# Kernel tuning notes

Measured on AMD Instinct MI355X. Metric: run time of the kernel, lower is better.

The kernel has to match this reference:

```python
import jax, jax.numpy as jnp
import numpy as np

NUM_CLASSES = 10
PGD_NUMS = 10
ALPHA = 0.15
# Hardcoded in the original module: sign vector for 10 classes
SIGN_VEC = jnp.array([-1.0] * 4 + [1.0] * 6, dtype=jnp.float32)


def setup_inputs() -> dict:
    key = jax.random.key(0)
    k1, k2, k3 = jax.random.split(key, 3)
    B = 1048576
    logit = jax.random.normal(k1, (B, NUM_CLASSES), dtype=jnp.float32)
    y = jax.random.randint(k2, (B,), 0, NUM_CLASSES, dtype=jnp.int32)
    label_freq = jax.random.randint(k3, (NUM_CLASSES,), 0, PGD_NUMS, dtype=jnp.int32)
    return {"logit": logit, "y": y, "label_freq": label_freq}


def _compute_adv(logit, y):
    # softmax over classes, then per-class mean of softmax rows (one-hot^T @ p)
    p = jax.nn.softmax(logit, axis=-1)  # [B, C]
    sum_class_logit = jax.ops.segment_sum(p, y, num_segments=NUM_CLASSES)  # [C, C]
    counts = jax.ops.segment_sum(jnp.ones(y.shape[0], dtype=logit.dtype), y,
                                 num_segments=NUM_CLASSES)  # [C]
    counts = jnp.where(counts == 0, jnp.asarray(100.0, logit.dtype), counts)
    mean_class_logit = sum_class_logit / counts[:, None]  # [C, C]
    grad = mean_class_logit - jnp.eye(NUM_CLASSES, dtype=logit.dtype)
    # Faithful to torch: norm over dim=0 (columns), then reshape(-1,1) divides row i
    col_norm = jnp.linalg.norm(grad, axis=0)  # [C]
    grad = grad / col_norm[:, None]
    grad = ALPHA * grad * SIGN_VEC[:, None].astype(logit.dtype)
    return grad[y]  # index_select along dim 0 -> [B, C]


def reference(logit, y, label_freq):
    logit_copy = logit

    def step(l, _):
        l_new = l + _compute_adv(l, y)
        return l_new, l_new

    _, logit_steps = jax.lax.scan(step, logit, None, length=PGD_NUMS)  # [P, B, C]

    # Original: logit_news = sum_i logit_steps[label_freq[i]] * (y == i)
    # Since class masks are disjoint, this is a per-sample gather of step label_freq[y[n]].
    steps_per_sample = label_freq[y]  # [B]
    B = logit.shape[0]
    logit_news = logit_steps[steps_per_sample, jnp.arange(B)]  # [B, C]

    # mean cross-entropy
    log_p = jax.nn.log_softmax(logit_news, axis=-1)
    loss_adv = -jnp.mean(jnp.take_along_axis(log_p, y[:, None].astype(jnp.int32), axis=1))
    return loss_adv, logit_news, logit_copy
```

## Files before the change

kernel.cpp:

```cpp
#include <hip/hip_runtime.h>
#include <hip/hip_cooperative_groups.h>

#define PGD   10
#define ALPHA 0.15f
#define NTAB  32
#define NSUB  8

#define FTH   512
#define FSP   4
#define FTS   (FTH * FSP)

#define NTHR  256
#define SPT   4
#define TSAMP (NTHR * SPT)

#define WS_COUNTS 0
#define WS_STAB   320
#define WS_DGLOB  32320
#define WS_BAR    33320
#define WS_ZERO_N 33324

__global__ void k_init(float* __restrict__ ws, float* __restrict__ out) {
    int i = blockIdx.x * blockDim.x + threadIdx.x;
    if (i == 0) out[0] = 0.f;
    int gs = gridDim.x * blockDim.x;
    for (int k = i; k < WS_ZERO_N; k += gs) ws[k] = 0.f;
}

__device__ __forceinline__ float aload(const float* p) {
    return __hip_atomic_load(p, __ATOMIC_RELAXED, __HIP_MEMORY_SCOPE_AGENT);
}

__device__ __forceinline__ void table_phase(
    const float* __restrict__ Sg, const float* __restrict__ counts_tab,
    const float* Dprev, float* shT, float* shCnt, float* shCn,
    float* shD_out, int tid)
{
    if (tid < 10) {
        float s = 0.f;
        #pragma unroll
        for (int k = 0; k < NTAB; ++k) s += counts_tab[k * 10 + tid];
        shCnt[tid] = (s == 0.f) ? 100.f : s;
    }
    if (tid < 100) {
        float s = 0.f;
        #pragma unroll
        for (int k = 0; k < NTAB; ++k) s += Sg[k * 100 + tid];
        shT[tid] = s;
    }
    __syncthreads();
    if (tid < 100) {
        int c = tid / 10, j = tid - c * 10;
        shT[tid] = shT[tid] / shCnt[c] - ((c == j) ? 1.f : 0.f);
    }
    __syncthreads();
    if (tid < 10) {
        float s = 0.f;
        for (int cc = 0; cc < 10; ++cc) { float g = shT[cc * 10 + tid]; s += g * g; }
        shCn[tid] = sqrtf(s);
    }
    __syncthreads();
    if (tid < 100) {
        int c = tid / 10;
        float sign = (c < 4) ? -1.f : 1.f;
        float g = shT[tid] / shCn[c] * (ALPHA * sign);
        shD_out[tid] = (Dprev ? Dprev[tid] : 0.f) + g;
    }
    __syncthreads();
}

__device__ __forceinline__ void load4(const float* __restrict__ logit,
                                      const int* __restrict__ y,
                                      int s0, int B, float* a, int* yc) {
    if (s0 + 4 <= B) {
        const float4* rp = reinterpret_cast<const float4*>(logit + (size_t)s0 * 10);
        float4 q[10];
        #pragma unroll
        for (int i = 0; i < 10; ++i) q[i] = rp[i];
        int4 yv = *reinterpret_cast<const int4*>(y + s0);
        #pragma unroll
        for (int i = 0; i < 10; ++i) {
            a[4 * i + 0] = q[i].x; a[4 * i + 1] = q[i].y;
            a[4 * i + 2] = q[i].z; a[4 * i + 3] = q[i].w;
        }
        yc[0] = yv.x; yc[1] = yv.y; yc[2] = yv.z; yc[3] = yv.w;
    } else {
        #pragma unroll
        for (int k = 0; k < 4; ++k) {
            int idx = s0 + k;
            if (idx < B) {
                yc[k] = y[idx];
                for (int j = 0; j < 10; ++j) a[k * 10 + j] = logit[(size_t)idx * 10 + j];
            } else {
                yc[k] = -1;
                for (int j = 0; j < 10; ++j) a[k * 10 + j] = 0.f;
            }
        }
    }
}

__global__ __launch_bounds__(FTH, 2) void k_fused(
    const float* __restrict__ logit, const int* __restrict__ y,
    const int* __restrict__ label_freq,
    float* __restrict__ out, float* __restrict__ ws, int B)
{
    __shared__ float tile[1024 * 10];
    __shared__ float Dall[PGD][100];
    __shared__ float shT[100];
    __shared__ float shCnt[10];
    __shared__ float shCn[10];
    __shared__ float wtab[NSUB][100];
    __shared__ float ctab[NSUB][10];
    __shared__ int   lf[10];
    __shared__ float wsum[8];

    const int tid = threadIdx.x;
    float* counts_tab = ws + WS_COUNTS;
    float* S_tab      = ws + WS_STAB;
    int*   bar        = (int*)(ws + WS_BAR);

    const size_t ftot = (size_t)B * 10;
    float* news_out = out + 1;
    float* copy_out = out + 1 + ftot;

    if (tid < 10) lf[tid] = label_freq[tid];

    const int s0 = (blockIdx.x * FTH + tid) * FSP;
    float a[40];
    int   yc[4];
    load4(logit, y, s0, B, a, yc);

    const size_t fbase = (size_t)blockIdx.x * (FTS * 10);
    #pragma unroll
    for (int i = 0; i < 10; ++i) {
        size_t fi = fbase + (size_t)(tid + i * FTH) * 4;
        if (fi + 4 <= ftot) {
            float4 v = *reinterpret_cast<const float4*>(logit + fi);
            *reinterpret_cast<float4*>(copy_out + fi) = v;
        } else {
            for (size_t e = fi; e < ftot; ++e) copy_out[e] = logit[e];
        }
    }

    const int nblk = gridDim.x;

    for (int t = 1; t <= PGD; ++t) {
        for (int i = tid; i < NSUB * 100; i += FTH) (&wtab[0][0])[i] = 0.f;
        if (t == 1) for (int i = tid; i < NSUB * 10; i += FTH) (&ctab[0][0])[i] = 0.f;
        __syncthreads();

        const int sub = ((tid >> 6) << 1) | (tid & 1);
        #pragma unroll
        for (int k = 0; k < FSP; ++k) {
            int c = yc[k];
            if (c < 0) continue;
            float tv[10];
            #pragma unroll
            for (int j = 0; j < 10; ++j) tv[j] = a[k * 10 + j];
            if (t >= 2) {
                #pragma unroll
                for (int j = 0; j < 10; ++j) tv[j] += Dall[t - 2][c * 10 + j];
            }
            float m = tv[0];
            #pragma unroll
            for (int j = 1; j < 10; ++j) m = fmaxf(m, tv[j]);
            float s = 0.f;
            #pragma unroll
            for (int j = 0; j < 10; ++j) { tv[j] = __expf(tv[j] - m); s += tv[j]; }
            float r = 1.f / s;
            #pragma unroll
            for (int j = 0; j < 10; ++j) unsafeAtomicAdd(&wtab[sub][c * 10 + j], tv[j] * r);
            if (t == 1) unsafeAtomicAdd(&ctab[sub][c], 1.f);
        }
        __syncthreads();

        const int tb = blockIdx.x & (NTAB - 1);
        if (tid < 100) {
            float s = 0.f;
            #pragma unroll
            for (int w = 0; w < NSUB; ++w) s += wtab[w][tid];
            atomicAdd(&S_tab[(size_t)(t - 1) * (NTAB * 100) + (size_t)tb * 100 + tid], s);
        }
        if (t == 1 && tid < 10) {
            float s = 0.f;
            #pragma unroll
            for (int w = 0; w < NSUB; ++w) s += ctab[w][tid];
            atomicAdd(&counts_tab[tb * 10 + tid], s);
        }

        __syncthreads();
        if (tid == 0) {
            __hip_atomic_fetch_add(bar, 1, __ATOMIC_ACQ_REL, __HIP_MEMORY_SCOPE_AGENT);
            while (__hip_atomic_load(bar, __ATOMIC_ACQUIRE, __HIP_MEMORY_SCOPE_AGENT) < nblk * t)
                __builtin_amdgcn_s_sleep(16);
        }
        __syncthreads();

        if (tid < 10) {
            float s = 0.f;
            #pragma unroll
            for (int k = 0; k < NTAB; ++k) s += aload(&counts_tab[k * 10 + tid]);
            shCnt[tid] = (s == 0.f) ? 100.f : s;
        }
        if (tid < 100) {
            float s = 0.f;
            const float* Sg = S_tab + (size_t)(t - 1) * (NTAB * 100);
            #pragma unroll
            for (int k = 0; k < NTAB; ++k) s += aload(&Sg[k * 100 + tid]);
            shT[tid] = s;
        }
        __syncthreads();
        if (tid < 100) {
            int c = tid / 10, j = tid - c * 10;
            shT[tid] = shT[tid] / shCnt[c] - ((c == j) ? 1.f : 0.f);
        }
        __syncthreads();
        if (tid < 10) {
            float s = 0.f;
            for (int cc = 0; cc < 10; ++cc) { float g = shT[cc * 10 + tid]; s += g * g; }
            shCn[tid] = sqrtf(s);
        }
        __syncthreads();
        if (tid < 100) {
            int c = tid / 10;
            float sign = (c < 4) ? -1.f : 1.f;
            float g = shT[tid] / shCn[c] * (ALPHA * sign);
            Dall[t - 1][tid] = ((t >= 2) ? Dall[t - 2][tid] : 0.f) + g;
        }
        __syncthreads();
    }

    float acc = 0.f;
    for (int cc = 0; cc < 2; ++cc) {
        __syncthreads();
        if ((tid >> 8) == cc) {
            const int lt = tid & 255;
            #pragma unroll
            for (int k = 0; k < FSP; ++k) {
                int c = yc[k];
                if (c < 0) continue;
                int rrel = lt * FSP + k;
                int sel = lf[c];
                float nv[10];
                #pragma unroll
                for (int j = 0; j < 10; ++j) nv[j] = a[k * 10 + j] + Dall[sel][c * 10 + j];
                #pragma unroll
                for (int j = 0; j < 10; ++j) tile[rrel * 10 + j] = nv[j];
                float m = nv[0];
                #pragma unroll
                for (int j = 1; j < 10; ++j) m = fmaxf(m, nv[j]);
                float s = 0.f;
                #pragma unroll
                for (int j = 0; j < 10; ++j) s += __expf(nv[j] - m);
                acc += __logf(s) + m - nv[c];
            }
        }
        __syncthreads();
        const float4* tp = reinterpret_cast<const float4*>(tile);
        #pragma unroll
        for (int i = 0; i < 5; ++i) {
            size_t fo = fbase + (size_t)cc * 10240 + (size_t)(tid + i * FTH) * 4;
            if (fo + 4 <= ftot) {
                *reinterpret_cast<float4*>(news_out + fo) = tp[tid + i * FTH];
            } else {
                size_t lbase = fbase + (size_t)cc * 10240;
                for (size_t e = fo; e < ftot; ++e) news_out[e] = tile[e - lbase];
            }
        }
    }

    #pragma unroll
    for (int off = 32; off > 0; off >>= 1) acc += __shfl_down(acc, off);
    if ((tid & 63) == 0) wsum[tid >> 6] = acc;
    __syncthreads();
    if (tid == 0) {
        float b = 0.f;
        #pragma unroll
        for (int w = 0; w < 8; ++w) b += wsum[w];
        atomicAdd(out, b / (float)B);
    }
}

__global__ __launch_bounds__(NTHR) void k_step(
    const float* __restrict__ logit, const int* __restrict__ y,
    float* __restrict__ ws, int B, int t)
{
    __shared__ float sh_D[100];
    __shared__ float shT[100];
    __shared__ float shCnt[10];
    __shared__ float shCn[10];
    __shared__ float wtab[NSUB][100];
    __shared__ float ctab[NSUB][10];

    const int tid = threadIdx.x;
    float* counts_tab = ws + WS_COUNTS;
    float* S_tab      = ws + WS_STAB;
    float* D_glob     = ws + WS_DGLOB;

    const int s0 = (blockIdx.x * NTHR + tid) * SPT;
    float a[40];
    int   yc[4];
    load4(logit, y, s0, B, a, yc);

    for (int i = tid; i < NSUB * 100; i += NTHR) (&wtab[0][0])[i] = 0.f;
    if (t == 1) for (int i = tid; i < NSUB * 10; i += NTHR) (&ctab[0][0])[i] = 0.f;

    if (t >= 2) {
        table_phase(S_tab + (size_t)(t - 2) * (NTAB * 100), counts_tab,
                    (t >= 3) ? (D_glob + (size_t)(t - 3) * 100) : nullptr,
                    shT, shCnt, shCn, sh_D, tid);
        if (blockIdx.x == 0 && tid < 100) D_glob[(size_t)(t - 2) * 100 + tid] = sh_D[tid];
    }
    __syncthreads();

    const int sub = ((tid >> 6) << 1) | (tid & 1);
    #pragma unroll
    for (int k = 0; k < SPT; ++k) {
        int c = yc[k];
        if (c < 0) continue;
        float tv[10];
        #pragma unroll
        for (int j = 0; j < 10; ++j) tv[j] = a[k * 10 + j];
        if (t >= 2) {
            #pragma unroll
            for (int j = 0; j < 10; ++j) tv[j] += sh_D[c * 10 + j];
        }
        float m = tv[0];
        #pragma unroll
        for (int j = 1; j < 10; ++j) m = fmaxf(m, tv[j]);
        float s = 0.f;
        #pragma unroll
        for (int j = 0; j < 10; ++j) { tv[j] = __expf(tv[j] - m); s += tv[j]; }
        float r = 1.f / s;
        #pragma unroll
        for (int j = 0; j < 10; ++j) unsafeAtomicAdd(&wtab[sub][c * 10 + j], tv[j] * r);
        if (t == 1) unsafeAtomicAdd(&ctab[sub][c], 1.f);
    }
    __syncthreads();

    const int tb = blockIdx.x & (NTAB - 1);
    if (tid < 100) {
        float s = 0.f;
        #pragma unroll
        for (int w = 0; w < NSUB; ++w) s += wtab[w][tid];
        unsafeAtomicAdd(&S_tab[(size_t)(t - 1) * (NTAB * 100) + (size_t)tb * 100 + tid], s);
    }
    if (t == 1 && tid < 10) {
        float s = 0.f;
        #pragma unroll
        for (int w = 0; w < NSUB; ++w) s += ctab[w][tid];
        unsafeAtomicAdd(&counts_tab[tb * 10 + tid], s);
    }
}

__global__ __launch_bounds__(NTHR) void k_final(
    const float* __restrict__ logit, const int* __restrict__ y,
    const int* __restrict__ label_freq,
    float* __restrict__ out, float* __restrict__ ws, int B)
{
    __shared__ float tile_f[TSAMP * 10];
    __shared__ int   yt[TSAMP];
    __shared__ float Dall[PGD][100];
    __shared__ float shT[100];
    __shared__ float shCnt[10];
    __shared__ float shCn[10];
    __shared__ int   lf[10];
    __shared__ float wsum[4];

    const int tid = threadIdx.x;
    float* counts_tab = ws + WS_COUNTS;
    float* S_tab      = ws + WS_STAB;
    float* D_glob     = ws + WS_DGLOB;

    const size_t fbase = (size_t)blockIdx.x * (TSAMP * 10);
    const size_t ftot  = (size_t)B * 10;
    float4 q[10];
    int4 yq;
    #pragma unroll
    for (int i = 0; i < 10; ++i) {
        size_t fi = fbase + (size_t)(tid + i * NTHR) * 4;
        if (fi + 4 <= ftot) {
            q[i] = *reinterpret_cast<const float4*>(logit + fi);
        } else {
            float e[4];
            #pragma unroll
            for (int e2 = 0; e2 < 4; ++e2) e[e2] = (fi + e2 < ftot) ? logit[fi + e2] : 0.f;
            q[i] = make_float4(e[0], e[1], e[2], e[3]);
        }
    }
    {
        int yi = blockIdx.x * TSAMP + tid * 4;
        if (yi + 4 <= B) {
            yq = *reinterpret_cast<const int4*>(y + yi);
        } else {
            yq.x = (yi < B) ? y[yi] : 0;
            yq.y = (yi + 1 < B) ? y[yi + 1] : 0;
            yq.z = (yi + 2 < B) ? y[yi + 2] : 0;
            yq.w = (yi + 3 < B) ? y[yi + 3] : 0;
        }
    }

    table_phase(S_tab + (size_t)9 * (NTAB * 100), counts_tab, D_glob + 8 * 100,
                shT, shCnt, shCn, &Dall[9][0], tid);
    for (int i = tid; i < 900; i += NTHR) Dall[i / 100][i % 100] = D_glob[i];
    if (tid < 10) lf[tid] = label_freq[tid];

    float4* tp = reinterpret_cast<float4*>(tile_f);
    #pragma unroll
    for (int i = 0; i < 10; ++i) tp[tid + i * NTHR] = q[i];
    reinterpret_cast<int4*>(yt)[tid] = yq;
    __syncthreads();

    const int vfloat = (int)((ftot - fbase < (size_t)(TSAMP * 10)) ? (ftot - fbase)
                                                                   : (size_t)(TSAMP * 10));
    float* news_out = out + 1;
    float* copy_out = out + 1 + ftot;

    for (int m = tid; m < vfloat; m += NTHR) copy_out[fbase + m] = tile_f[m];
    __syncthreads();

    float acc = 0.f;
    #pragma unroll
    for (int k = 0; k < SPT; ++k) {
        int sl = tid + k * NTHR;
        int gi = blockIdx.x * TSAMP + sl;
        if (gi >= B) break;
        int c = yt[sl];
        int sel = lf[c];
        float2* rp = reinterpret_cast<float2*>(tile_f + sl * 10);
        float nv[10];
        #pragma unroll
        for (int h = 0; h < 5; ++h) {
            float2 v = rp[h];
            nv[2 * h]     = v.x + Dall[sel][c * 10 + 2 * h];
            nv[2 * h + 1] = v.y + Dall[sel][c * 10 + 2 * h + 1];
        }
        #pragma unroll
        for (int h = 0; h < 5; ++h) rp[h] = make_float2(nv[2 * h], nv[2 * h + 1]);
        float m = nv[0];
        #pragma unroll
        for (int j = 1; j < 10; ++j) m = fmaxf(m, nv[j]);
        float s = 0.f;
        #pragma unroll
        for (int j = 0; j < 10; ++j) s += __expf(nv[j] - m);
        acc += __logf(s) + m - nv[c];
    }
    __syncthreads();

    for (int m = tid; m < vfloat; m += NTHR) news_out[fbase + m] = tile_f[m];

    #pragma unroll
    for (int off = 32; off > 0; off >>= 1) acc += __shfl_down(acc, off);
    if ((tid & 63) == 0) wsum[tid >> 6] = acc;
    __syncthreads();
    if (tid == 0)
        unsafeAtomicAdd(out, (wsum[0] + wsum[1] + wsum[2] + wsum[3]) / (float)B);
}

extern "C" void kernel_launch(void* const* d_in, const int* in_sizes, int n_in,
                              void* d_out, int out_size, void* d_ws, size_t ws_size,
                              hipStream_t stream) {
    const float* logit = (const float*)d_in[0];
    const int*   yy    = (const int*)d_in[1];
    const int*   lf    = (const int*)d_in[2];
    float* out = (float*)d_out;
    float* ws  = (float*)d_ws;
    int B = in_sizes[0] / 10;

    int fblocks = (B + FTS - 1) / FTS;

    int dev = 0; hipGetDevice(&dev);
    int numCU = 0;
    hipDeviceGetAttribute(&numCU, hipDeviceAttributeMultiprocessorCount, dev);
    int maxB = 0;
    hipOccupancyMaxActiveBlocksPerMultiprocessor(&maxB, (const void*)k_fused, FTH, 0);
    bool coop_ok = (maxB > 0) && ((long)maxB * (long)numCU >= (long)fblocks);

    hipLaunchKernelGGL(k_init, dim3(64), dim3(256), 0, stream, ws, out);

    if (coop_ok) {
        void* args[] = { (void*)&logit, (void*)&yy, (void*)&lf,
                         (void*)&out, (void*)&ws, (void*)&B };
        hipLaunchCooperativeKernel((const void*)k_fused, dim3(fblocks), dim3(FTH),
                                   args, 0, stream);
    } else {
        int blocks = (B + TSAMP - 1) / TSAMP;
        for (int t = 1; t <= PGD; ++t)
            hipLaunchKernelGGL(k_step, dim3(blocks), dim3(NTHR), 0, stream,
                               logit, yy, ws, B, t);
        hipLaunchKernelGGL(k_final, dim3(blocks), dim3(NTHR), 0, stream,
                           logit, yy, lf, out, ws, B);
    }
}
```

Baseline: 645.4 us.

## Double samples per thread and replace global barrier with master-reduce broadcast

Each thread now holds 8 samples instead of 4, which halves the grid size and so the number of blocks taking part in each grid-wide synchronization. The single contended barrier counter is replaced by 32 padded arrival counters. Block 0 alone waits on them, reduces the per-step tables, computes the step delta and publishes it to global memory with a release flag, while the other blocks spin on that flag and copy the delta. This targets barrier contention and redundant per-block reductions, at the cost of much higher register pressure (80 floats per thread), which may cause spills or lower occupancy, and one serialized block on the critical path.

```diff
diff --git a/kernel.cpp b/kernel.cpp
--- a/kernel.cpp
+++ b/kernel.cpp
@@ -7,7 +7,7 @@
 #define NSUB  8
 
 #define FTH   512
-#define FSP   4
+#define FSP   8
 #define FTS   (FTH * FSP)
 
 #define NTHR  256
@@ -17,8 +17,9 @@
 #define WS_COUNTS 0
 #define WS_STAB   320
 #define WS_DGLOB  32320
-#define WS_BAR    33320
-#define WS_ZERO_N 33324
+#define WS_ARR    33320
+#define WS_REL    33832
+#define WS_ZERO_N 33840
 
 __global__ void k_init(float* __restrict__ ws, float* __restrict__ out) {
     int i = blockIdx.x * blockDim.x + threadIdx.x;
@@ -117,7 +118,9 @@
     const int tid = threadIdx.x;
     float* counts_tab = ws + WS_COUNTS;
     float* S_tab      = ws + WS_STAB;
-    int*   bar        = (int*)(ws + WS_BAR);
+    float* D_glob     = ws + WS_DGLOB;
+    int*   arr        = (int*)(ws + WS_ARR);
+    int*   rel        = (int*)(ws + WS_REL);
 
     const size_t ftot = (size_t)B * 10;
     float* news_out = out + 1;
@@ -126,13 +129,14 @@
     if (tid < 10) lf[tid] = label_freq[tid];
 
     const int s0 = (blockIdx.x * FTH + tid) * FSP;
-    float a[40];
-    int   yc[4];
-    load4(logit, y, s0, B, a, yc);
+    float a[80];
+    int   yc[8];
+    load4(logit, y, s0,     B, a,      yc);
+    load4(logit, y, s0 + 4, B, a + 40, yc + 4);
 
     const size_t fbase = (size_t)blockIdx.x * (FTS * 10);
     #pragma unroll
-    for (int i = 0; i < 10; ++i) {
+    for (int i = 0; i < 20; ++i) {
         size_t fi = fbase + (size_t)(tid + i * FTH) * 4;
         if (fi + 4 <= ftot) {
             float4 v = *reinterpret_cast<const float4*>(logit + fi);
@@ -187,54 +191,80 @@
             for (int w = 0; w < NSUB; ++w) s += ctab[w][tid];
             atomicAdd(&counts_tab[tb * 10 + tid], s);
         }
-
         __syncthreads();
-        if (tid == 0) {
-            __hip_atomic_fetch_add(bar, 1, __ATOMIC_ACQ_REL, __HIP_MEMORY_SCOPE_AGENT);
-            while (__hip_atomic_load(bar, __ATOMIC_ACQUIRE, __HIP_MEMORY_SCOPE_AGENT) < nblk * t)
-                __builtin_amdgcn_s_sleep(16);
-        }
+
+        if (tid == 0)
+            __hip_atomic_fetch_add(&arr[(blockIdx.x & 31) * 16], 1,
+                                   __ATOMIC_RELEASE, __HIP_MEMORY_SCOPE_AGENT);
+
+        if (blockIdx.x == 0) {
+            if (tid == 0) {
+                for (;;) {
+                    int s = 0;
+                    #pragma unroll
+                    for (int i = 0; i < 32; ++i)
+                        s += __hip_atomic_load(&arr[i * 16], __ATOMIC_ACQUIRE,
+                                               __HIP_MEMORY_SCOPE_AGENT);
+                    if (s >= nblk * t) break;
+                    __builtin_amdgcn_s_sleep(8);
+                }
+            }
+            __syncthreads();
+            if (t == 1 && tid < 10) {
+                float s = 0.f;
+                #pragma unroll
+                for (int k = 0; k < NTAB; ++k) s += aload(&counts_tab[k * 10 + tid]);
+                shCnt[tid] = (s == 0.f) ? 100.f : s;
+            }
+            if (tid < 100) {
+                float s = 0.f;
+                const float* Sg = S_tab + (size_t)(t - 1) * (NTAB * 100);
+                #pragma unroll
+                for (int k = 0; k < NTAB; ++k) s += aload(&Sg[k * 100 + tid]);
+                shT[tid] = s;
+            }
+            __syncthreads();
+            if (tid < 100) {
+                int c = tid / 10, j = tid - c * 10;
+                shT[tid] = shT[tid] / shCnt[c] - ((c == j) ? 1.f : 0.f);
+            }
+            __syncthreads();
+            if (tid < 10) {
+                float s = 0.f;
+                for (int cc = 0; cc < 10; ++cc) { float g = shT[cc * 10 + tid]; s += g * g; }
+                shCn[tid] = sqrtf(s);
+            }
+            __syncthreads();
+            if (tid < 100) {
+                int c = tid / 10;
+                float sign = (c < 4) ? -1.f : 1.f;
+                float g = shT[tid] / shCn[c] * (ALPHA * sign);
+                float d = ((t >= 2) ? Dall[t - 2][tid] : 0.f) + g;
+                Dall[t - 1][tid] = d;
+                __hip_atomic_store(&D_glob[(size_t)(t - 1) * 100 + tid], d,
+                                   __ATOMIC_RELEASE, __HIP_MEMORY_SCOPE_AGENT);
+            }
+            __syncthreads();
+            if (tid == 0)
+                __hip_atomic_store(rel, t, __ATOMIC_RELEASE, __HIP_MEMORY_SCOPE_AGENT);
+        } else {
+            if (tid == 0) {
+                while (__hip_atomic_load(rel, __ATOMIC_ACQUIRE,
+                                         __HIP_MEMORY_SCOPE_AGENT) < t)
+                    __builtin_amdgcn_s_sleep(8);
+            }
+            __syncthreads();
+            if (tid < 100)
+                Dall[t - 1][tid] = aload(&D_glob[(size_t)(t - 1) * 100 + tid]);
+            __syncthreads();
+        }
+    }
+
+    float acc = 0.f;
+    for (int cc = 0; cc < 4; ++cc) {
         __syncthreads();
-
-        if (tid < 10) {
-            float s = 0.f;
-            #pragma unroll
-            for (int k = 0; k < NTAB; ++k) s += aload(&counts_tab[k * 10 + tid]);
-            shCnt[tid] = (s == 0.f) ? 100.f : s;
-        }
-        if (tid < 100) {
-            float s = 0.f;
-            const float* Sg = S_tab + (size_t)(t - 1) * (NTAB * 100);
-            #pragma unroll
-            for (int k = 0; k < NTAB; ++k) s += aload(&Sg[k * 100 + tid]);
-            shT[tid] = s;
-        }
-        __syncthreads();
-        if (tid < 100) {
-            int c = tid / 10, j = tid - c * 10;
-            shT[tid] = shT[tid] / shCnt[c] - ((c == j) ? 1.f : 0.f);
-        }
-        __syncthreads();
-        if (tid < 10) {
-            float s = 0.f;
-            for (int cc = 0; cc < 10; ++cc) { float g = shT[cc * 10 + tid]; s += g * g; }
-            shCn[tid] = sqrtf(s);
-        }
-        __syncthreads();
-        if (tid < 100) {
-            int c = tid / 10;
-            float sign = (c < 4) ? -1.f : 1.f;
-            float g = shT[tid] / shCn[c] * (ALPHA * sign);
-            Dall[t - 1][tid] = ((t >= 2) ? Dall[t - 2][tid] : 0.f) + g;
-        }
-        __syncthreads();
-    }
-
-    float acc = 0.f;
-    for (int cc = 0; cc < 2; ++cc) {
-        __syncthreads();
-        if ((tid >> 8) == cc) {
-            const int lt = tid & 255;
+        if ((tid >> 7) == cc) {
+            const int lt = tid & 127;
             #pragma unroll
             for (int k = 0; k < FSP; ++k) {
                 int c = yc[k];
```

After: 646.8 us. About the same (+0.2%).
